# Kernel optimization log

Hardware: AMD Instinct MI355X
Metric: run time of the kernel (lower is better)

## Reference

```python
import jax, jax.numpy as jnp
import numpy as np

ENC_H, DEC_H, ATTN = 1024, 1024, 512
B, S = 32, 4096


def setup_inputs() -> dict:
    key = jax.random.key(0)
    k1, k2, k3, k4, k5, k6 = jax.random.split(key, 6)
    decoder_state = jax.random.normal(k1, (B, DEC_H), dtype=jnp.float32)
    encoder_outputs = jax.random.normal(k2, (B, S, ENC_H), dtype=jnp.float32)
    mask = jax.random.randint(k3, (B, S), 0, 2, dtype=jnp.int32)
    W_h = jax.random.normal(k4, (ENC_H, ATTN), dtype=jnp.float32) / np.sqrt(ENC_H)
    W_s = jax.random.normal(k5, (DEC_H, ATTN), dtype=jnp.float32) / np.sqrt(DEC_H)
    v = jax.random.normal(k6, (ATTN,), dtype=jnp.float32) / np.sqrt(ATTN)
    return {"decoder_state": decoder_state, "encoder_outputs": encoder_outputs,
            "mask": mask, "W_h": W_h, "W_s": W_s, "v": v}


def reference(decoder_state, encoder_outputs, mask, W_h, W_s, v):
    # proj_enc: (B, S, A), proj_dec: (B, 1, A)
    proj_enc = jnp.einsum('bse,ea->bsa', encoder_outputs, W_h)
    proj_dec = jnp.einsum('bd,da->ba', decoder_state, W_s)[:, None, :]
    # scores: (B, S) = v^T tanh(W_h h_j + W_s s_i)
    scores = jnp.einsum('bsa,a->bs', jnp.tanh(proj_enc + proj_dec), v)
    neg_inf = jnp.finfo(scores.dtype).min
    scores = jnp.where(mask == 0, neg_inf, scores)
    weights = jax.nn.softmax(scores, axis=-1)  # (B, S)
    context = jnp.einsum('bs,bse->be', weights, encoder_outputs)  # (B, ENC_H)
    return context, weights
```

## Files before the change

kernel.cpp:

```cpp
#include <hip/hip_runtime.h>
#include <hip/hip_bf16.h>
#include <float.h>
#include <math.h>

#define NB 32
#define NS 4096
#define NE 1024
#define ND 1024
#define NA 512

typedef __attribute__((ext_vector_type(4))) float f32x4;
typedef __attribute__((ext_vector_type(8))) short short8;

static __device__ __forceinline__ ushort f2bf(float f){
    union { float f; unsigned int u; } x; x.f = f;
    unsigned int u = x.u + 0x7fffu + ((x.u >> 16) & 1u);
    return (ushort)(u >> 16);
}

static __device__ __forceinline__ float tanh_fast(float x){
    float e = __expf(2.f * x);
    return 1.f - 2.f / (e + 1.f);
}

__global__ __launch_bounds__(256) void k_prep_wtf(const float* __restrict__ Wh,
                                                  ushort* __restrict__ WTf){
    int i = blockIdx.x * 256 + threadIdx.x;
    int e = i & 7;
    int lane = (i >> 3) & 63;
    int ng = (i >> 9) & 31;
    int s = i >> 14;
    int k = s * 32 + (lane >> 4) * 8 + e;
    int col = ng * 16 + (lane & 15);
    WTf[i] = f2bf(Wh[k * NA + col]);
}

__global__ __launch_bounds__(512) void k_projdec(const float* __restrict__ dec,
                                                 const float* __restrict__ Ws,
                                                 float* __restrict__ pdp){
    int b = blockIdx.x >> 2, kc = blockIdx.x & 3;
    int a = threadIdx.x;
    const float* dp = dec + b * ND + kc * 256;
    const float* wp = Ws + (size_t)(kc * 256) * NA + a;
    float acc = 0.f;
    #pragma unroll 4
    for (int k = 0; k < 256; k++) acc += dp[k] * wp[(size_t)k * NA];
    pdp[(kc * NB + b) * NA + a] = acc;
}

__global__ __launch_bounds__(256, 4) void k_scores(const float* __restrict__ E,
                                                   const ushort* __restrict__ WTf,
                                                   const float* __restrict__ pdp,
                                                   const float* __restrict__ v,
                                                   float* __restrict__ scrp){
    const int t = threadIdx.x;
    const int lane = t & 63, w = t >> 6;
    const int l15 = lane & 15, grp = lane >> 4;
    const int wm = w >> 1, wn = w & 1;

    const int bid = blockIdx.x;
    const int xcd = bid & 7, slot = bid >> 3;
    const int mblk = xcd * 128 + (slot >> 2);
    const int bn = slot & 3;
    const int m0 = mblk << 7;
    const int b = mblk >> 5;

    __shared__ __align__(16) ushort bft[2][128 * 32];
    __shared__ float sc[128][2];

    const int sr = t >> 1, half = t & 1;
    const float* gsrc = E + (size_t)(m0 + sr) * NE + half * 16;

    f32x4 acc[4][4];
    f32x4 zero; zero[0]=0.f; zero[1]=0.f; zero[2]=0.f; zero[3]=0.f;
    #pragma unroll
    for (int m = 0; m < 4; m++)
        #pragma unroll
        for (int n = 0; n < 4; n++) acc[m][n] = zero;

    f32x4 st[4];
    auto stage_load = [&](int it){
        const f32x4* p = (const f32x4*)(gsrc + it * 32);
        st[0] = p[0]; st[1] = p[1]; st[2] = p[2]; st[3] = p[3];
    };
    auto stage_write = [&](int buf){
        short8 h0, h1;
        #pragma unroll
        for (int e = 0; e < 4; e++){
            h0[e]     = (short)__builtin_bit_cast(ushort, __float2bfloat16(st[0][e]));
            h0[e + 4] = (short)__builtin_bit_cast(ushort, __float2bfloat16(st[1][e]));
            h1[e]     = (short)__builtin_bit_cast(ushort, __float2bfloat16(st[2][e]));
            h1[e + 4] = (short)__builtin_bit_cast(ushort, __float2bfloat16(st[3][e]));
        }
        char* bb = (char*)&bft[buf][0];
        unsigned s0 = (unsigned)(half * 2);
        *(short8*)(bb + sr * 64 + (((s0    ) ^ (unsigned)(sr & 3)) << 4)) = h0;
        *(short8*)(bb + sr * 64 + (((s0 + 1) ^ (unsigned)(sr & 3)) << 4)) = h1;
    };

    const ushort* wtf0 = WTf + ((size_t)(bn * 8 + wn * 4) * 64 + lane) * 8;

    stage_load(0);
    stage_write(0);
    asm volatile("s_waitcnt lgkmcnt(0)" ::: "memory");
    __builtin_amdgcn_s_barrier();

    for (int it = 0; it < 32; ++it){
        const int buf = it & 1;
        short8 wt[4];
        const ushort* wp = wtf0 + (size_t)it * 16384;
        #pragma unroll
        for (int n = 0; n < 4; n++) wt[n] = *(const short8*)(wp + n * 512);
        __builtin_amdgcn_sched_barrier(0);
        if (it < 31) stage_load(it + 1);
        __builtin_amdgcn_sched_barrier(0);
        const char* base = (const char*)&bft[buf][0];
        #pragma unroll
        for (int m = 0; m < 4; m++){
            const int r = wm * 64 + m * 16 + l15;
            short8 af = *(const short8*)(base + r * 64 + (((unsigned)grp ^ (unsigned)(r & 3)) << 4));
            #pragma unroll
            for (int n = 0; n < 4; n++)
                acc[m][n] = __builtin_amdgcn_mfma_f32_16x16x32_bf16(af, wt[n], acc[m][n], 0, 0, 0);
        }
        __builtin_amdgcn_sched_barrier(0);
        if (it < 31) stage_write(buf ^ 1);
        asm volatile("s_waitcnt lgkmcnt(0)" ::: "memory");
        __builtin_amdgcn_s_barrier();
    }

    float pdc[4], vc[4];
    #pragma unroll
    for (int n = 0; n < 4; n++){
        int c = bn * 128 + wn * 64 + n * 16 + l15;
        float p = 0.f;
        #pragma unroll
        for (int kc = 0; kc < 4; kc++) p += pdp[(kc * NB + b) * NA + c];
        pdc[n] = p;
        vc[n] = v[c];
    }
    #pragma unroll
    for (int m = 0; m < 4; m++){
        #pragma unroll
        for (int j = 0; j < 4; j++){
            float s = 0.f;
            #pragma unroll
            for (int n = 0; n < 4; n++) s += tanh_fast(acc[m][n][j] + pdc[n]) * vc[n];
            s += __shfl_xor(s, 1);
            s += __shfl_xor(s, 2);
            s += __shfl_xor(s, 4);
            s += __shfl_xor(s, 8);
            if (l15 == 0) sc[wm * 64 + m * 16 + grp * 4 + j][wn] = s;
        }
    }
    __syncthreads();
    if (t < 128)
        scrp[(size_t)bn * (NB * NS) + m0 + t] = sc[t][0] + sc[t][1];
}

__global__ __launch_bounds__(256) void k_softmax(const float* __restrict__ scrp,
                                                 const int* __restrict__ mask,
                                                 float* __restrict__ weights){
    int b = blockIdx.x, t = threadIdx.x;
    __shared__ float red[8];
    float vals[16];
    float mx = -FLT_MAX;
    #pragma unroll
    for (int i = 0; i < 16; i++){
        int s = i * 256 + t;
        float x = scrp[b * NS + s]
                + scrp[(size_t)(NB * NS) + b * NS + s]
                + scrp[2 * (size_t)(NB * NS) + b * NS + s]
                + scrp[3 * (size_t)(NB * NS) + b * NS + s];
        x = (mask[b * NS + s] != 0) ? x : -FLT_MAX;
        vals[i] = x;
        mx = fmaxf(mx, x);
    }
    #pragma unroll
    for (int off = 32; off; off >>= 1) mx = fmaxf(mx, __shfl_xor(mx, off));
    int wv = t >> 6;
    if ((t & 63) == 0) red[wv] = mx;
    __syncthreads();
    mx = fmaxf(fmaxf(red[0], red[1]), fmaxf(red[2], red[3]));
    float sum = 0.f;
    #pragma unroll
    for (int i = 0; i < 16; i++){ vals[i] = __expf(vals[i] - mx); sum += vals[i]; }
    #pragma unroll
    for (int off = 32; off; off >>= 1) sum += __shfl_xor(sum, off);
    if ((t & 63) == 0) red[4 + wv] = sum;
    __syncthreads();
    sum = red[4] + red[5] + red[6] + red[7];
    float inv = 1.f / sum;
    #pragma unroll
    for (int i = 0; i < 16; i++) weights[b * NS + i * 256 + t] = vals[i] * inv;
}

__global__ __launch_bounds__(1024) void k_context(const float* __restrict__ E,
                                                  const float* __restrict__ weights,
                                                  float* __restrict__ part){
    int b = blockIdx.x >> 3, ch = blockIdx.x & 7;
    int t = threadIdx.x;
    int h = t >> 8, tg = t & 255;
    __shared__ float wsm[512];
    __shared__ __align__(16) f32x4 red[4][256];
    if (t < 512) wsm[t] = weights[b * NS + ch * 512 + t];
    __syncthreads();
    const f32x4* Ep = (const f32x4*)(E + ((size_t)b * NS + ch * 512 + h * 128) * NE) + tg;
    f32x4 acc; acc[0]=0.f; acc[1]=0.f; acc[2]=0.f; acc[3]=0.f;
    #pragma unroll 4
    for (int s = 0; s < 128; s++){
        f32x4 e = Ep[(size_t)s * 256];
        float w = wsm[h * 128 + s];
        acc[0] += w * e[0]; acc[1] += w * e[1];
        acc[2] += w * e[2]; acc[3] += w * e[3];
    }
    red[h][tg] = acc;
    __syncthreads();
    if (h == 0){
        f32x4 a0 = red[0][tg], a1 = red[1][tg], a2 = red[2][tg], a3 = red[3][tg];
        f32x4 s;
        s[0] = a0[0]+a1[0]+a2[0]+a3[0];
        s[1] = a0[1]+a1[1]+a2[1]+a3[1];
        s[2] = a0[2]+a1[2]+a2[2]+a3[2];
        s[3] = a0[3]+a1[3]+a2[3]+a3[3];
        *(f32x4*)(part + ((size_t)(b * 8 + ch)) * NE + tg * 4) = s;
    }
}

__global__ __launch_bounds__(256) void k_reduce_ctx(const float* __restrict__ part,
                                                    float* __restrict__ ctx){
    int i = blockIdx.x * 256 + threadIdx.x;
    int b = i >> 10, e = i & 1023;
    float s = 0.f;
    #pragma unroll
    for (int ch = 0; ch < 8; ch++) s += part[((size_t)(b * 8 + ch)) * NE + e];
    ctx[i] = s;
}

extern "C" void kernel_launch(void* const* d_in, const int* in_sizes, int n_in,
                              void* d_out, int out_size, void* d_ws, size_t ws_size,
                              hipStream_t stream){
    const float* dec  = (const float*)d_in[0];
    const float* E    = (const float*)d_in[1];
    const int*   mask = (const int*)d_in[2];
    const float* Wh   = (const float*)d_in[3];
    const float* Ws   = (const float*)d_in[4];
    const float* v    = (const float*)d_in[5];
    float* ctx = (float*)d_out;
    float* weights = (float*)d_out + NB * NE;

    char* ws = (char*)d_ws;
    ushort* WTf  = (ushort*)ws;
    float*  part = (float*)ws;
    float*  pdp  = (float*)(ws + (1 << 20));
    float*  scrp = (float*)(ws + (1 << 20) + (256 << 10));

    k_prep_wtf<<<2048, 256, 0, stream>>>(Wh, WTf);
    k_projdec<<<128, 512, 0, stream>>>(dec, Ws, pdp);
    k_scores<<<4096, 256, 0, stream>>>(E, WTf, pdp, v, scrp);
    k_softmax<<<32, 256, 0, stream>>>(scrp, mask, weights);
    k_context<<<256, 1024, 0, stream>>>(E, weights, part);
    k_reduce_ctx<<<128, 256, 0, stream>>>(part, ctx);
}
```

Measured before the change: 369.2 us.

## Load encoder A-fragments directly from global memory, dropping LDS staging

```diff
diff --git a/kernel.cpp b/kernel.cpp
--- a/kernel.cpp
+++ b/kernel.cpp
@@ -48,7 +48,7 @@
     pdp[(kc * NB + b) * NA + a] = acc;
 }
 
-__global__ __launch_bounds__(256, 4) void k_scores(const float* __restrict__ E,
+__global__ __launch_bounds__(256, 3) void k_scores(const float* __restrict__ E,
                                                    const ushort* __restrict__ WTf,
                                                    const float* __restrict__ pdp,
                                                    const float* __restrict__ v,
@@ -65,11 +65,7 @@
     const int m0 = mblk << 7;
     const int b = mblk >> 5;
 
-    __shared__ __align__(16) ushort bft[2][128 * 32];
     __shared__ float sc[128][2];
-
-    const int sr = t >> 1, half = t & 1;
-    const float* gsrc = E + (size_t)(m0 + sr) * NE + half * 16;
 
     f32x4 acc[4][4];
     f32x4 zero; zero[0]=0.f; zero[1]=0.f; zero[2]=0.f; zero[3]=0.f;
@@ -78,55 +74,37 @@
         #pragma unroll
         for (int n = 0; n < 4; n++) acc[m][n] = zero;
 
-    f32x4 st[4];
-    auto stage_load = [&](int it){
-        const f32x4* p = (const f32x4*)(gsrc + it * 32);
-        st[0] = p[0]; st[1] = p[1]; st[2] = p[2]; st[3] = p[3];
-    };
-    auto stage_write = [&](int buf){
-        short8 h0, h1;
-        #pragma unroll
-        for (int e = 0; e < 4; e++){
-            h0[e]     = (short)__builtin_bit_cast(ushort, __float2bfloat16(st[0][e]));
-            h0[e + 4] = (short)__builtin_bit_cast(ushort, __float2bfloat16(st[1][e]));
-            h1[e]     = (short)__builtin_bit_cast(ushort, __float2bfloat16(st[2][e]));
-            h1[e + 4] = (short)__builtin_bit_cast(ushort, __float2bfloat16(st[3][e]));
-        }
-        char* bb = (char*)&bft[buf][0];
-        unsigned s0 = (unsigned)(half * 2);
-        *(short8*)(bb + sr * 64 + (((s0    ) ^ (unsigned)(sr & 3)) << 4)) = h0;
-        *(short8*)(bb + sr * 64 + (((s0 + 1) ^ (unsigned)(sr & 3)) << 4)) = h1;
-    };
+    const float* am[4];
+    #pragma unroll
+    for (int m = 0; m < 4; m++)
+        am[m] = E + (size_t)(m0 + wm * 64 + m * 16 + l15) * NE + grp * 8;
 
     const ushort* wtf0 = WTf + ((size_t)(bn * 8 + wn * 4) * 64 + lane) * 8;
 
-    stage_load(0);
-    stage_write(0);
-    asm volatile("s_waitcnt lgkmcnt(0)" ::: "memory");
-    __builtin_amdgcn_s_barrier();
-
     for (int it = 0; it < 32; ++it){
-        const int buf = it & 1;
         short8 wt[4];
         const ushort* wp = wtf0 + (size_t)it * 16384;
         #pragma unroll
         for (int n = 0; n < 4; n++) wt[n] = *(const short8*)(wp + n * 512);
-        __builtin_amdgcn_sched_barrier(0);
-        if (it < 31) stage_load(it + 1);
-        __builtin_amdgcn_sched_barrier(0);
-        const char* base = (const char*)&bft[buf][0];
+        f32x4 a0[4], a1[4];
         #pragma unroll
         for (int m = 0; m < 4; m++){
-            const int r = wm * 64 + m * 16 + l15;
-            short8 af = *(const short8*)(base + r * 64 + (((unsigned)grp ^ (unsigned)(r & 3)) << 4));
+            const float* p = am[m] + it * 32;
+            a0[m] = *(const f32x4*)p;
+            a1[m] = *(const f32x4*)(p + 4);
+        }
+        #pragma unroll
+        for (int m = 0; m < 4; m++){
+            short8 af;
+            #pragma unroll
+            for (int e = 0; e < 4; e++){
+                af[e]     = (short)__builtin_bit_cast(ushort, __float2bfloat16(a0[m][e]));
+                af[e + 4] = (short)__builtin_bit_cast(ushort, __float2bfloat16(a1[m][e]));
+            }
             #pragma unroll
             for (int n = 0; n < 4; n++)
                 acc[m][n] = __builtin_amdgcn_mfma_f32_16x16x32_bf16(af, wt[n], acc[m][n], 0, 0, 0);
         }
-        __builtin_amdgcn_sched_barrier(0);
-        if (it < 31) stage_write(buf ^ 1);
-        asm volatile("s_waitcnt lgkmcnt(0)" ::: "memory");
-        __builtin_amdgcn_s_barrier();
     }
 
     float pdc[4], vc[4];
```

New measurement: 681.2 us. 1.85x slower.

## Pre-convert encoder outputs to bf16 and stream them into LDS via direct DMA

Applied to the files above, without the earlier changes.

```diff
diff --git a/kernel.cpp b/kernel.cpp
--- a/kernel.cpp
+++ b/kernel.cpp
@@ -11,11 +11,19 @@
 
 typedef __attribute__((ext_vector_type(4))) float f32x4;
 typedef __attribute__((ext_vector_type(8))) short short8;
+typedef __attribute__((ext_vector_type(4))) ushort ushort4v;
+typedef __attribute__((address_space(3))) char lds_char_t;
+typedef __attribute__((address_space(1))) const char g_char_t;
 
 static __device__ __forceinline__ ushort f2bf(float f){
     union { float f; unsigned int u; } x; x.f = f;
     unsigned int u = x.u + 0x7fffu + ((x.u >> 16) & 1u);
     return (ushort)(u >> 16);
+}
+
+static __device__ __forceinline__ float bf2f(ushort h){
+    union { unsigned int u; float f; } x; x.u = ((unsigned int)h) << 16;
+    return x.f;
 }
 
 static __device__ __forceinline__ float tanh_fast(float x){
@@ -48,11 +56,28 @@
     pdp[(kc * NB + b) * NA + a] = acc;
 }
 
-__global__ __launch_bounds__(256, 4) void k_scores(const float* __restrict__ E,
-                                                   const ushort* __restrict__ WTf,
-                                                   const float* __restrict__ pdp,
-                                                   const float* __restrict__ v,
-                                                   float* __restrict__ scrp){
+__global__ __launch_bounds__(256) void k_cvt_e(const float* __restrict__ E,
+                                               ushort* __restrict__ E16){
+    const size_t nchunks = (size_t)NB * NS * NE / 8;
+    const size_t stride = (size_t)gridDim.x * 256;
+    for (size_t c = (size_t)blockIdx.x * 256 + threadIdx.x; c < nchunks; c += stride){
+        const f32x4* p = (const f32x4*)(E + c * 8);
+        f32x4 lo = p[0], hi = p[1];
+        short8 h;
+        #pragma unroll
+        for (int e = 0; e < 4; e++){
+            h[e]     = (short)f2bf(lo[e]);
+            h[e + 4] = (short)f2bf(hi[e]);
+        }
+        *(short8*)(E16 + c * 8) = h;
+    }
+}
+
+__global__ __launch_bounds__(256, 3) void k_scores16(const ushort* __restrict__ E16,
+                                                     const ushort* __restrict__ WTf,
+                                                     const float* __restrict__ pdp,
+                                                     const float* __restrict__ v,
+                                                     float* __restrict__ scrp){
     const int t = threadIdx.x;
     const int lane = t & 63, w = t >> 6;
     const int l15 = lane & 15, grp = lane >> 4;
@@ -65,11 +90,21 @@
     const int m0 = mblk << 7;
     const int b = mblk >> 5;
 
-    __shared__ __align__(16) ushort bft[2][128 * 32];
+    __shared__ __align__(16) ushort ring[3][128 * 64];
     __shared__ float sc[128][2];
 
-    const int sr = t >> 1, half = t & 1;
-    const float* gsrc = E + (size_t)(m0 + sr) * NE + half * 16;
+    auto dma = [&](int it){
+        char* bufp = (char*)&ring[it % 3][0];
+        #pragma unroll
+        for (int j = 0; j < 4; ++j){
+            const int c = (w * 4 + j) * 64 + lane;
+            const int row = c >> 3, q = c & 7;
+            const int qs = q ^ (row & 7);
+            const ushort* src = E16 + (size_t)(m0 + row) * NE + it * 64 + qs * 8;
+            __builtin_amdgcn_global_load_lds((g_char_t*)src,
+                                             (lds_char_t*)(bufp + c * 16), 16, 0, 0);
+        }
+    };
 
     f32x4 acc[4][4];
     f32x4 zero; zero[0]=0.f; zero[1]=0.f; zero[2]=0.f; zero[3]=0.f;
@@ -78,55 +113,41 @@
         #pragma unroll
         for (int n = 0; n < 4; n++) acc[m][n] = zero;
 
-    f32x4 st[4];
-    auto stage_load = [&](int it){
-        const f32x4* p = (const f32x4*)(gsrc + it * 32);
-        st[0] = p[0]; st[1] = p[1]; st[2] = p[2]; st[3] = p[3];
-    };
-    auto stage_write = [&](int buf){
-        short8 h0, h1;
-        #pragma unroll
-        for (int e = 0; e < 4; e++){
-            h0[e]     = (short)__builtin_bit_cast(ushort, __float2bfloat16(st[0][e]));
-            h0[e + 4] = (short)__builtin_bit_cast(ushort, __float2bfloat16(st[1][e]));
-            h1[e]     = (short)__builtin_bit_cast(ushort, __float2bfloat16(st[2][e]));
-            h1[e + 4] = (short)__builtin_bit_cast(ushort, __float2bfloat16(st[3][e]));
-        }
-        char* bb = (char*)&bft[buf][0];
-        unsigned s0 = (unsigned)(half * 2);
-        *(short8*)(bb + sr * 64 + (((s0    ) ^ (unsigned)(sr & 3)) << 4)) = h0;
-        *(short8*)(bb + sr * 64 + (((s0 + 1) ^ (unsigned)(sr & 3)) << 4)) = h1;
-    };
-
     const ushort* wtf0 = WTf + ((size_t)(bn * 8 + wn * 4) * 64 + lane) * 8;
 
-    stage_load(0);
-    stage_write(0);
-    asm volatile("s_waitcnt lgkmcnt(0)" ::: "memory");
+    dma(0);
+    dma(1);
+    asm volatile("s_waitcnt vmcnt(4)" ::: "memory");
     __builtin_amdgcn_s_barrier();
 
-    for (int it = 0; it < 32; ++it){
-        const int buf = it & 1;
-        short8 wt[4];
-        const ushort* wp = wtf0 + (size_t)it * 16384;
-        #pragma unroll
-        for (int n = 0; n < 4; n++) wt[n] = *(const short8*)(wp + n * 512);
-        __builtin_amdgcn_sched_barrier(0);
-        if (it < 31) stage_load(it + 1);
-        __builtin_amdgcn_sched_barrier(0);
-        const char* base = (const char*)&bft[buf][0];
-        #pragma unroll
-        for (int m = 0; m < 4; m++){
-            const int r = wm * 64 + m * 16 + l15;
-            short8 af = *(const short8*)(base + r * 64 + (((unsigned)grp ^ (unsigned)(r & 3)) << 4));
+    for (int it = 0; it < 16; ++it){
+        short8 wt0[4], wt1[4];
+        const ushort* wp = wtf0 + (size_t)(2 * it) * 16384;
+        #pragma unroll
+        for (int n = 0; n < 4; n++) wt0[n] = *(const short8*)(wp + n * 512);
+        #pragma unroll
+        for (int n = 0; n < 4; n++) wt1[n] = *(const short8*)(wp + 16384 + n * 512);
+        __builtin_amdgcn_sched_barrier(0);
+        if (it < 14) dma(it + 2);
+        __builtin_amdgcn_sched_barrier(0);
+        const char* base = (const char*)&ring[it % 3][0];
+        #pragma unroll
+        for (int kk = 0; kk < 2; kk++){
             #pragma unroll
-            for (int n = 0; n < 4; n++)
-                acc[m][n] = __builtin_amdgcn_mfma_f32_16x16x32_bf16(af, wt[n], acc[m][n], 0, 0, 0);
-        }
-        __builtin_amdgcn_sched_barrier(0);
-        if (it < 31) stage_write(buf ^ 1);
-        asm volatile("s_waitcnt lgkmcnt(0)" ::: "memory");
-        __builtin_amdgcn_s_barrier();
+            for (int m = 0; m < 4; m++){
+                const int r = wm * 64 + m * 16 + l15;
+                short8 af = *(const short8*)(base + r * 128 + (((kk * 4 + grp) ^ (r & 7)) << 4));
+                short8* wtk = kk ? wt1 : wt0;
+                #pragma unroll
+                for (int n = 0; n < 4; n++)
+                    acc[m][n] = __builtin_amdgcn_mfma_f32_16x16x32_bf16(af, wtk[n], acc[m][n], 0, 0, 0);
+            }
+        }
+        __builtin_amdgcn_sched_barrier(0);
+        if (it < 15){
+            asm volatile("s_waitcnt vmcnt(4)" ::: "memory");
+            __builtin_amdgcn_s_barrier();
+        }
     }
 
     float pdc[4], vc[4];
@@ -158,6 +179,179 @@
         scrp[(size_t)bn * (NB * NS) + m0 + t] = sc[t][0] + sc[t][1];
 }
 
+__global__ __launch_bounds__(1024) void k_context16(const ushort* __restrict__ E16,
+                                                    const float* __restrict__ weights,
+                                                    float* __restrict__ part){
+    int b = blockIdx.x >> 3, ch = blockIdx.x & 7;
+    int t = threadIdx.x;
+    int h = t >> 8, tg = t & 255;
+    __shared__ float wsm[512];
+    __shared__ __align__(16) f32x4 red[4][256];
+    if (t < 512) wsm[t] = weights[b * NS + ch * 512 + t];
+    __syncthreads();
+    const ushort* Ep = E16 + ((size_t)b * NS + ch * 512 + h * 128) * NE + tg * 4;
+    f32x4 acc; acc[0]=0.f; acc[1]=0.f; acc[2]=0.f; acc[3]=0.f;
+    #pragma unroll 4
+    for (int s = 0; s < 128; s++){
+        ushort4v u = *(const ushort4v*)(Ep + (size_t)s * NE);
+        float w = wsm[h * 128 + s];
+        acc[0] += w * bf2f(u[0]); acc[1] += w * bf2f(u[1]);
+        acc[2] += w * bf2f(u[2]); acc[3] += w * bf2f(u[3]);
+    }
+    red[h][tg] = acc;
+    __syncthreads();
+    if (h == 0){
+        f32x4 a0 = red[0][tg], a1 = red[1][tg], a2 = red[2][tg], a3 = red[3][tg];
+        f32x4 s;
+        s[0] = a0[0]+a1[0]+a2[0]+a3[0];
+        s[1] = a0[1]+a1[1]+a2[1]+a3[1];
+        s[2] = a0[2]+a1[2]+a2[2]+a3[2];
+        s[3] = a0[3]+a1[3]+a2[3]+a3[3];
+        *(f32x4*)(part + ((size_t)(b * 8 + ch)) * NE + tg * 4) = s;
+    }
+}
+
+__global__ __launch_bounds__(256, 3) void k_scores(const float* __restrict__ E,
+                                                   const ushort* __restrict__ WTf,
+                                                   const float* __restrict__ pdp,
+                                                   const float* __restrict__ v,
+                                                   float* __restrict__ scrp){
+    const int t = threadIdx.x;
+    const int lane = t & 63, w = t >> 6;
+    const int l15 = lane & 15, grp = lane >> 4;
+    const int wm = w >> 1, wn = w & 1;
+    const int bid = blockIdx.x;
+    const int xcd = bid & 7, slot = bid >> 3;
+    const int mblk = xcd * 128 + (slot >> 2);
+    const int bn = slot & 3;
+    const int m0 = mblk << 7;
+    const int b = mblk >> 5;
+
+    __shared__ __align__(16) ushort bft[2][128 * 32];
+    __shared__ float sc[128][2];
+
+    const int sr = t >> 1, half = t & 1;
+    const float* gsrc = E + (size_t)(m0 + sr) * NE + half * 16;
+
+    f32x4 acc[4][4];
+    f32x4 zero; zero[0]=0.f; zero[1]=0.f; zero[2]=0.f; zero[3]=0.f;
+    #pragma unroll
+    for (int m = 0; m < 4; m++)
+        #pragma unroll
+        for (int n = 0; n < 4; n++) acc[m][n] = zero;
+
+    f32x4 st[4];
+    auto stage_load = [&](int it){
+        const f32x4* p = (const f32x4*)(gsrc + it * 32);
+        st[0] = p[0]; st[1] = p[1]; st[2] = p[2]; st[3] = p[3];
+    };
+    auto stage_write = [&](int buf){
+        short8 h0, h1;
+        #pragma unroll
+        for (int e = 0; e < 4; e++){
+            h0[e]     = (short)f2bf(st[0][e]);
+            h0[e + 4] = (short)f2bf(st[1][e]);
+            h1[e]     = (short)f2bf(st[2][e]);
+            h1[e + 4] = (short)f2bf(st[3][e]);
+        }
+        char* bb = (char*)&bft[buf][0];
+        unsigned s0 = (unsigned)(half * 2);
+        *(short8*)(bb + sr * 64 + (((s0    ) ^ (unsigned)(sr & 3)) << 4)) = h0;
+        *(short8*)(bb + sr * 64 + (((s0 + 1) ^ (unsigned)(sr & 3)) << 4)) = h1;
+    };
+
+    const ushort* wtf0 = WTf + ((size_t)(bn * 8 + wn * 4) * 64 + lane) * 8;
+
+    stage_load(0);
+    stage_write(0);
+    asm volatile("s_waitcnt lgkmcnt(0)" ::: "memory");
+    __builtin_amdgcn_s_barrier();
+
+    for (int it = 0; it < 32; ++it){
+        const int buf = it & 1;
+        short8 wt[4];
+        const ushort* wp = wtf0 + (size_t)it * 16384;
+        #pragma unroll
+        for (int n = 0; n < 4; n++) wt[n] = *(const short8*)(wp + n * 512);
+        __builtin_amdgcn_sched_barrier(0);
+        if (it < 31) stage_load(it + 1);
+        __builtin_amdgcn_sched_barrier(0);
+        const char* base = (const char*)&bft[buf][0];
+        #pragma unroll
+        for (int m = 0; m < 4; m++){
+            const int r = wm * 64 + m * 16 + l15;
+            short8 af = *(const short8*)(base + r * 64 + (((unsigned)grp ^ (unsigned)(r & 3)) << 4));
+            #pragma unroll
+            for (int n = 0; n < 4; n++)
+                acc[m][n] = __builtin_amdgcn_mfma_f32_16x16x32_bf16(af, wt[n], acc[m][n], 0, 0, 0);
+        }
+        __builtin_amdgcn_sched_barrier(0);
+        if (it < 31) stage_write(buf ^ 1);
+        asm volatile("s_waitcnt lgkmcnt(0)" ::: "memory");
+        __builtin_amdgcn_s_barrier();
+    }
+
+    float pdc[4], vc[4];
+    #pragma unroll
+    for (int n = 0; n < 4; n++){
+        int c = bn * 128 + wn * 64 + n * 16 + l15;
+        float p = 0.f;
+        #pragma unroll
+        for (int kc = 0; kc < 4; kc++) p += pdp[(kc * NB + b) * NA + c];
+        pdc[n] = p;
+        vc[n] = v[c];
+    }
+    #pragma unroll
+    for (int m = 0; m < 4; m++){
+        #pragma unroll
+        for (int j = 0; j < 4; j++){
+            float s = 0.f;
+            #pragma unroll
+            for (int n = 0; n < 4; n++) s += tanh_fast(acc[m][n][j] + pdc[n]) * vc[n];
+            s += __shfl_xor(s, 1);
+            s += __shfl_xor(s, 2);
+            s += __shfl_xor(s, 4);
+            s += __shfl_xor(s, 8);
+            if (l15 == 0) sc[wm * 64 + m * 16 + grp * 4 + j][wn] = s;
+        }
+    }
+    __syncthreads();
+    if (t < 128)
+        scrp[(size_t)bn * (NB * NS) + m0 + t] = sc[t][0] + sc[t][1];
+}
+
+__global__ __launch_bounds__(1024) void k_context(const float* __restrict__ E,
+                                                  const float* __restrict__ weights,
+                                                  float* __restrict__ part){
+    int b = blockIdx.x >> 3, ch = blockIdx.x & 7;
+    int t = threadIdx.x;
+    int h = t >> 8, tg = t & 255;
+    __shared__ float wsm[512];
+    __shared__ __align__(16) f32x4 red[4][256];
+    if (t < 512) wsm[t] = weights[b * NS + ch * 512 + t];
+    __syncthreads();
+    const f32x4* Ep = (const f32x4*)(E + ((size_t)b * NS + ch * 512 + h * 128) * NE) + tg;
+    f32x4 acc; acc[0]=0.f; acc[1]=0.f; acc[2]=0.f; acc[3]=0.f;
+    #pragma unroll 4
+    for (int s = 0; s < 128; s++){
+        f32x4 e = Ep[(size_t)s * 256];
+        float w = wsm[h * 128 + s];
+        acc[0] += w * e[0]; acc[1] += w * e[1];
+        acc[2] += w * e[2]; acc[3] += w * e[3];
+    }
+    red[h][tg] = acc;
+    __syncthreads();
+    if (h == 0){
+        f32x4 a0 = red[0][tg], a1 = red[1][tg], a2 = red[2][tg], a3 = red[3][tg];
+        f32x4 s;
+        s[0] = a0[0]+a1[0]+a2[0]+a3[0];
+        s[1] = a0[1]+a1[1]+a2[1]+a3[1];
+        s[2] = a0[2]+a1[2]+a2[2]+a3[2];
+        s[3] = a0[3]+a1[3]+a2[3]+a3[3];
+        *(f32x4*)(part + ((size_t)(b * 8 + ch)) * NE + tg * 4) = s;
+    }
+}
+
 __global__ __launch_bounds__(256) void k_softmax(const float* __restrict__ scrp,
                                                  const int* __restrict__ mask,
                                                  float* __restrict__ weights){
@@ -193,38 +387,6 @@
     float inv = 1.f / sum;
     #pragma unroll
     for (int i = 0; i < 16; i++) weights[b * NS + i * 256 + t] = vals[i] * inv;
-}
-
-__global__ __launch_bounds__(1024) void k_context(const float* __restrict__ E,
-                                                  const float* __restrict__ weights,
-                                                  float* __restrict__ part){
-    int b = blockIdx.x >> 3, ch = blockIdx.x & 7;
-    int t = threadIdx.x;
-    int h = t >> 8, tg = t & 255;
-    __shared__ float wsm[512];
-    __shared__ __align__(16) f32x4 red[4][256];
-    if (t < 512) wsm[t] = weights[b * NS + ch * 512 + t];
-    __syncthreads();
-    const f32x4* Ep = (const f32x4*)(E + ((size_t)b * NS + ch * 512 + h * 128) * NE) + tg;
-    f32x4 acc; acc[0]=0.f; acc[1]=0.f; acc[2]=0.f; acc[3]=0.f;
-    #pragma unroll 4
-    for (int s = 0; s < 128; s++){
-        f32x4 e = Ep[(size_t)s * 256];
-        float w = wsm[h * 128 + s];
-        acc[0] += w * e[0]; acc[1] += w * e[1];
-        acc[2] += w * e[2]; acc[3] += w * e[3];
-    }
-    red[h][tg] = acc;
-    __syncthreads();
-    if (h == 0){
-        f32x4 a0 = red[0][tg], a1 = red[1][tg], a2 = red[2][tg], a3 = red[3][tg];
-        f32x4 s;
-        s[0] = a0[0]+a1[0]+a2[0]+a3[0];
-        s[1] = a0[1]+a1[1]+a2[1]+a3[1];
-        s[2] = a0[2]+a1[2]+a2[2]+a3[2];
-        s[3] = a0[3]+a1[3]+a2[3]+a3[3];
-        *(f32x4*)(part + ((size_t)(b * 8 + ch)) * NE + tg * 4) = s;
-    }
 }
 
 __global__ __launch_bounds__(256) void k_reduce_ctx(const float* __restrict__ part,
@@ -250,15 +412,34 @@
     float* weights = (float*)d_out + NB * NE;
 
     char* ws = (char*)d_ws;
-    ushort* WTf  = (ushort*)ws;
-    float*  part = (float*)ws;
-    float*  pdp  = (float*)(ws + (1 << 20));
-    float*  scrp = (float*)(ws + (1 << 20) + (256 << 10));
-
-    k_prep_wtf<<<2048, 256, 0, stream>>>(Wh, WTf);
-    k_projdec<<<128, 512, 0, stream>>>(dec, Ws, pdp);
-    k_scores<<<4096, 256, 0, stream>>>(E, WTf, pdp, v, scrp);
-    k_softmax<<<32, 256, 0, stream>>>(scrp, mask, weights);
-    k_context<<<256, 1024, 0, stream>>>(E, weights, part);
-    k_reduce_ctx<<<128, 256, 0, stream>>>(part, ctx);
-}
+    const size_t e16_bytes  = (size_t)NB * NS * NE * 2;
+    const size_t need = e16_bytes + (1 << 20) + (256 << 10) + (2 << 20) + (1 << 20);
+
+    if (ws_size >= need){
+        ushort* E16  = (ushort*)ws;
+        ushort* WTf  = (ushort*)(ws + e16_bytes);
+        float*  pdp  = (float*)(ws + e16_bytes + (1 << 20));
+        float*  scrp = (float*)(ws + e16_bytes + (1 << 20) + (256 << 10));
+        float*  part = (float*)(ws + e16_bytes + (1 << 20) + (256 << 10) + (2 << 20));
+
+        k_prep_wtf<<<2048, 256, 0, stream>>>(Wh, WTf);
+        k_projdec<<<128, 512, 0, stream>>>(dec, Ws, pdp);
+        k_cvt_e<<<4096, 256, 0, stream>>>(E, E16);
+        k_scores16<<<4096, 256, 0, stream>>>(E16, WTf, pdp, v, scrp);
+        k_softmax<<<32, 256, 0, stream>>>(scrp, mask, weights);
+        k_context16<<<256, 1024, 0, stream>>>(E16, weights, part);
+        k_reduce_ctx<<<128, 256, 0, stream>>>(part, ctx);
+    } else {
+        ushort* WTf  = (ushort*)ws;
+        float*  part = (float*)ws;
+        float*  pdp  = (float*)(ws + (1 << 20));
+        float*  scrp = (float*)(ws + (1 << 20) + (256 << 10));
+
+        k_prep_wtf<<<2048, 256, 0, stream>>>(Wh, WTf);
+        k_projdec<<<128, 512, 0, stream>>>(dec, Ws, pdp);
+        k_scores<<<4096, 256, 0, stream>>>(E, WTf, pdp, v, scrp);
+        k_softmax<<<32, 256, 0, stream>>>(scrp, mask, weights);
+        k_context<<<256, 1024, 0, stream>>>(E, weights, part);
+        k_reduce_ctx<<<128, 256, 0, stream>>>(part, ctx);
+    }
+}
```

Result: slower. 409.4 us (+10.9%).
